# Kernel tuning notes

Measured on AMD Instinct MI355X. Metric: run time of the kernel, lower is better.

The kernel has to match this reference:

```python
import jax, jax.numpy as jnp
import numpy as np

N, E, H, B = 100000, 1600000, 64, 256
EPS = 1e-5


def ln(x, g, b):
    mu = jnp.mean(x, axis=-1, keepdims=True)
    var = jnp.mean((x - mu) ** 2, axis=-1, keepdims=True)
    return (x - mu) * jax.lax.rsqrt(var + EPS) * g + b


def gelu(x):
    # torch nn.GELU default is exact (erf) gelu
    return jax.nn.gelu(x, approximate=False)


def setup_inputs() -> dict:
    key = jax.random.key(0)
    ks = iter(jax.random.split(key, 64))
    nk = lambda: next(ks)
    s = 0.1
    p = {}
    p["x"] = jax.random.normal(nk(), (N, 2), jnp.float32)
    p["edge_attr"] = jax.random.normal(nk(), (E, 2), jnp.float32)
    # node_embed: Linear(2,H) LN GELU Linear(H,H) LN GELU (dropout = eval no-op)
    p["ne_w1"] = jax.random.normal(nk(), (2, H), jnp.float32) * s
    p["ne_b1"] = jnp.zeros((H,), jnp.float32)
    p["ne_g1"] = jnp.ones((H,), jnp.float32)
    p["ne_be1"] = jnp.zeros((H,), jnp.float32)
    p["ne_w2"] = jax.random.normal(nk(), (H, H), jnp.float32) * s
    p["ne_b2"] = jnp.zeros((H,), jnp.float32)
    p["ne_g2"] = jnp.ones((H,), jnp.float32)
    p["ne_be2"] = jnp.zeros((H,), jnp.float32)
    # 3 TrackConv layers: message MLP Linear(H+2,H)+LN, conv output LN, and outer per-layer LN
    p["conv_w"] = jax.random.normal(nk(), (3, H + 2, H), jnp.float32) * s
    p["conv_b"] = jnp.zeros((3, H), jnp.float32)
    p["conv_mg"] = jnp.ones((3, H), jnp.float32)
    p["conv_mb"] = jnp.zeros((3, H), jnp.float32)
    p["conv_ng"] = jnp.ones((3, H), jnp.float32)
    p["conv_nb"] = jnp.zeros((3, H), jnp.float32)
    p["out_ng"] = jnp.ones((3, H), jnp.float32)
    p["out_nb"] = jnp.zeros((3, H), jnp.float32)
    # head MLP: Linear(H,H)+LN+ReLU, Linear(H,H//2)+LN+ReLU, Linear(H//2,1)
    p["m_w1"] = jax.random.normal(nk(), (H, H), jnp.float32) * s
    p["m_b1"] = jnp.zeros((H,), jnp.float32)
    p["m_g1"] = jnp.ones((H,), jnp.float32)
    p["m_be1"] = jnp.zeros((H,), jnp.float32)
    p["m_w2"] = jax.random.normal(nk(), (H, H // 2), jnp.float32) * s
    p["m_b2"] = jnp.zeros((H // 2,), jnp.float32)
    p["m_g2"] = jnp.ones((H // 2,), jnp.float32)
    p["m_be2"] = jnp.zeros((H // 2,), jnp.float32)
    p["m_w3"] = jax.random.normal(nk(), (H // 2, 1), jnp.float32) * s
    p["m_b3"] = jnp.zeros((1,), jnp.float32)
    p["edge_index"] = jax.random.randint(nk(), (2, E), 0, N, dtype=jnp.int32)
    p["batch"] = jnp.sort(jax.random.randint(nk(), (N,), 0, B, dtype=jnp.int32))
    return p


def reference(x, edge_attr,
              ne_w1, ne_b1, ne_g1, ne_be1, ne_w2, ne_b2, ne_g2, ne_be2,
              conv_w, conv_b, conv_mg, conv_mb, conv_ng, conv_nb, out_ng, out_nb,
              m_w1, m_b1, m_g1, m_be1, m_w2, m_b2, m_g2, m_be2, m_w3, m_b3,
              edge_index, batch):
    # node embedding (dropout in eval = identity)
    h = gelu(ln(x @ ne_w1 + ne_b1, ne_g1, ne_be1))
    h = gelu(ln(h @ ne_w2 + ne_b2, ne_g2, ne_be2))
    src, dst = edge_index[0], edge_index[1]  # PyG: message from src (x_j), aggregate at dst
    deg = jax.ops.segment_sum(jnp.ones((E,), h.dtype), dst, num_segments=N)
    deg = jnp.maximum(deg, 1.0)[:, None]
    for l in range(3):
        msg_in = jnp.concatenate([h[src], edge_attr], axis=-1)  # [E, H+2]
        msg = gelu(ln(msg_in @ conv_w[l] + conv_b[l], conv_mg[l], conv_mb[l]))  # [E, H]
        agg = jax.ops.segment_sum(msg, dst, num_segments=N) / deg  # mean aggregate
        conv_out = ln(agg + h, conv_ng[l], conv_nb[l])  # TrackConv: norm(out + residual)
        h = h + ln(conv_out, out_ng[l], out_nb[l])  # outer norm + residual
    # global mean pool over graphs
    cnt = jnp.maximum(jax.ops.segment_sum(jnp.ones((N,), h.dtype), batch, num_segments=B), 1.0)[:, None]
    g = jax.ops.segment_sum(h, batch, num_segments=B) / cnt  # [B, H]
    g = jax.nn.relu(ln(g @ m_w1 + m_b1, m_g1, m_be1))
    g = jax.nn.relu(ln(g @ m_w2 + m_b2, m_g2, m_be2))
    return g @ m_w3 + m_b3  # [B, 1]
```

## Files before the change

kernel.cpp:

```cpp
#include <hip/hip_runtime.h>
#include <math.h>


typedef __attribute__((ext_vector_type(8))) short bfrag;
typedef __attribute__((ext_vector_type(4))) float ffrag;

template <int CTRL>
__device__ __forceinline__ float dpp_mov(float v) {
  return __int_as_float(
      __builtin_amdgcn_update_dpp(0, __float_as_int(v), CTRL, 0xF, 0xF, true));
}

__device__ __forceinline__ float rsum16(float v) {
  v += dpp_mov<0x128>(v);
  v += dpp_mov<0x124>(v);
  v += dpp_mov<0x122>(v);
  v += dpp_mov<0x121>(v);
  return v;
}

__device__ __forceinline__ float wave_sum64(float v) {
  v = rsum16(v);
  v += __shfl_xor(v, 16, 64);
  v += __shfl_xor(v, 32, 64);
  return v;
}

__device__ __forceinline__ float ln_apply(float t, float g, float b) {
  float s1 = wave_sum64(t);
  float s2 = wave_sum64(t * t);
  float mu = s1 * 0.015625f;
  float var = fmaf(-mu, mu, s2 * 0.015625f);
  return (t - mu) * rsqrtf(var + 1e-5f) * g + b;
}

__device__ __forceinline__ float erf_fast(float x) {
  float ax = fabsf(x);
  float p = fmaf(fmaf(fmaf(fmaf(0.078108f, ax, 0.000972f), ax, 0.230389f),
                      ax, 0.278393f), ax, 1.0f);
  p = p * p;
  p = p * p;
  float r = __builtin_amdgcn_rcpf(p);
  return copysignf(1.0f - r, x);
}

__device__ __forceinline__ float gelu_exact(float v) {
  float half = 0.5f * v;
  return fmaf(half, erf_fast(v * 0.70710678118654752440f), half);
}

__device__ __forceinline__ float lane_bcast(float v, int k) {
  return __uint_as_float(__builtin_amdgcn_readlane(__float_as_uint(v), k));
}

__device__ __forceinline__ short f2bf(float f) {
  union { float f; unsigned u; } v; v.f = f;
  unsigned r = v.u + 0x7fffu + ((v.u >> 16) & 1u);
  return (short)(r >> 16);
}

__global__ __launch_bounds__(256) void k_init(
    const float* __restrict__ x,
    const float* __restrict__ w1, const float* __restrict__ b1,
    const float* __restrict__ g1, const float* __restrict__ be1,
    const float* __restrict__ w2, const float* __restrict__ b2,
    const float* __restrict__ g2, const float* __restrict__ be2,
    const float* __restrict__ conv_w, ushort* __restrict__ wt,
    const int* __restrict__ ei, int* __restrict__ csr,
    float* __restrict__ h, ushort* __restrict__ hb,
    int n_nodes, int ne, int oHist, int oEmb, int embWaves) {
  const int bid = blockIdx.x;
  const int tid = threadIdx.x;
  if (bid < oHist) {
    const int i = bid * 256 + tid;
    const int k = i % 96, f = (i / 96) % 64, l = i / (96 * 64);
    const float v = (k < 66) ? conv_w[(size_t)l * 66 * 64 + k * 64 + f] : 0.0f;
    wt[i] = (ushort)f2bf(v);
    return;
  }
  if (bid < oEmb) {
    const int i = (bid - oHist) * 256 + tid;
    if (i < ne) atomicAdd(&csr[ei[ne + i]], 1);
    return;
  }
  const int lane = tid & 63;
  const int wid = ((bid - oEmb) * 256 + tid) >> 6;
  const int nw = embWaves;
  float wc[64];
#pragma unroll
  for (int k = 0; k < 64; k++) wc[k] = w2[k * 64 + lane];
  const float w1a = w1[lane], w1b = w1[64 + lane];
  const float vb1 = b1[lane], vg1 = g1[lane], vbe1 = be1[lane];
  const float vb2 = b2[lane], vg2 = g2[lane], vbe2 = be2[lane];
  for (int n = wid; n < n_nodes; n += nw) {
    const float x0 = x[2 * n], x1 = x[2 * n + 1];
    float t = fmaf(x0, w1a, fmaf(x1, w1b, vb1));
    t = gelu_exact(ln_apply(t, vg1, vbe1));
    float a0 = vb2, a1 = 0.f, a2 = 0.f, a3 = 0.f;
#pragma unroll
    for (int k = 0; k < 64; k += 4) {
      a0 = fmaf(lane_bcast(t, k + 0), wc[k + 0], a0);
      a1 = fmaf(lane_bcast(t, k + 1), wc[k + 1], a1);
      a2 = fmaf(lane_bcast(t, k + 2), wc[k + 2], a2);
      a3 = fmaf(lane_bcast(t, k + 3), wc[k + 3], a3);
    }
    float acc = (a0 + a1) + (a2 + a3);
    acc = gelu_exact(ln_apply(acc, vg2, vbe2));
    h[n * 64 + lane] = acc;
    hb[n * 64 + lane] = (ushort)f2bf(acc);
  }
}

__global__ __launch_bounds__(1024) void k_scan_fast(int* __restrict__ buf, int n) {
  __shared__ int wsum[16];
  const int tid = threadIdx.x, lane = tid & 63, w = tid >> 6;
  const int chunk = (((n + 1023) / 1024) + 3) & ~3;
  const int a = min(tid * chunk, n), b = min(a + chunk, n);
  const bool full = (a + chunk <= n);
  int s = 0;
  if (full) {
    const int4* p4 = (const int4*)(buf + a);
#pragma unroll 4
    for (int i = 0; i < chunk / 4; i++) {
      int4 v = p4[i];
      s += v.x + v.y + v.z + v.w;
    }
  } else {
    for (int i = a; i < b; i++) s += buf[i];
  }
  int inc = s;
#pragma unroll
  for (int sh = 1; sh < 64; sh <<= 1) {
    int t = __shfl_up(inc, sh, 64);
    if (lane >= sh) inc += t;
  }
  if (lane == 63) wsum[w] = inc;
  __syncthreads();
  int wb = 0;
  for (int j = 0; j < w; j++) wb += wsum[j];
  int excl = wb + inc - s;
  if (full) {
    int4* p4 = (int4*)(buf + a);
#pragma unroll 4
    for (int i = 0; i < chunk / 4; i++) {
      int4 v = p4[i];
      int4 o;
      o.x = excl; excl += v.x;
      o.y = excl; excl += v.y;
      o.z = excl; excl += v.z;
      o.w = excl; excl += v.w;
      p4[i] = o;
    }
  } else {
    for (int i = a; i < b; i++) { int v = buf[i]; buf[i] = excl; excl += v; }
  }
}

__global__ void k_scatter(const int* __restrict__ ei, const float* __restrict__ ea,
                          int* __restrict__ cursor, int2* __restrict__ edata, int ne) {
  int i = blockIdx.x * blockDim.x + threadIdx.x;
  if (i < ne) {
    const int d = ei[ne + i];
    const int s = ei[i];
    const float2 eav = *(const float2*)(ea + 2 * (size_t)i);
    const unsigned pk = (unsigned)(ushort)f2bf(eav.x) |
                        ((unsigned)(ushort)f2bf(eav.y) << 16);
    const int pos = atomicAdd(&cursor[d], 1);
    edata[pos] = make_int2(s, (int)pk);
  }
}

__global__ __launch_bounds__(256, 3) void k_edge_node(
    const float* __restrict__ h_in, const ushort* __restrict__ hb_in,
    float* __restrict__ h_out, ushort* __restrict__ hb_out,
    const int2* __restrict__ edata, const int* __restrict__ ends,
    const ushort* __restrict__ wt,
    const float* __restrict__ bias, const float* __restrict__ mg,
    const float* __restrict__ mb,
    const float* __restrict__ ng, const float* __restrict__ nb,
    const float* __restrict__ og, const float* __restrict__ ob,
    int n_nodes, int writeHb) {
  __shared__ __align__(16) ushort lwt[64 * 96];
  {
    const uint4* s = (const uint4*)wt;
    uint4* d = (uint4*)lwt;
    for (int i = threadIdx.x; i < 768; i += 256) d[i] = s[i];
  }
  __syncthreads();

  const int lane = threadIdx.x & 63;
  const int grp = lane >> 4, col = lane & 15;
  const int wid = (blockIdx.x * blockDim.x + threadIdx.x) >> 6;
  const int nw = (gridDim.x * blockDim.x) >> 6;

  float vb[4], vg[4], vbb[4];
#pragma unroll
  for (int t = 0; t < 4; t++) {
    const int f = t * 16 + col;
    vb[t] = bias[f]; vg[t] = mg[f]; vbb[t] = mb[f];
  }

  for (int n = wid; n < n_nodes; n += nw) {
    int start, end;
    if (n == 0) {
      start = 0; end = ends[0];
    } else {
      const int2 se = *(const int2*)(ends + n - 1);
      start = se.x; end = se.y;
    }
    float aggf[4] = {0.f, 0.f, 0.f, 0.f};

    int p = start;
    int2 ed = edata[p + min(col, end - p - 1)];
    const ushort* hp0 = hb_in + (size_t)ed.x * 64 + grp * 8;
    bfrag A0 = *(const bfrag*)(hp0);
    bfrag A1 = *(const bfrag*)(hp0 + 32);
    int edy = ed.y;

    for (;;) {
      const int rem = min(16, end - p);
      const int pn = p + 16;
      const bool more = pn < end;
      const int nidx = more ? (pn + min(col, end - pn - 1)) : (p + min(col, rem - 1));
      const int2 edn = edata[nidx];

      bfrag A2 = {0, 0, 0, 0, 0, 0, 0, 0};
      if (grp == 0) {
        A2[0] = (short)(edy & 0xffff);
        A2[1] = (short)((unsigned)edy >> 16);
      }

      ffrag acc[4];
#pragma unroll
      for (int t = 0; t < 4; t++) { ffrag c = {vb[t], vb[t], vb[t], vb[t]}; acc[t] = c; }
#pragma unroll
      for (int t = 0; t < 4; t++) {
        const bfrag B = *(const bfrag*)(lwt + (t * 16 + col) * 96 + grp * 8);
        acc[t] = __builtin_amdgcn_mfma_f32_16x16x32_bf16(A0, B, acc[t], 0, 0, 0);
      }
#pragma unroll
      for (int t = 0; t < 4; t++) {
        const bfrag B = *(const bfrag*)(lwt + (t * 16 + col) * 96 + 32 + grp * 8);
        acc[t] = __builtin_amdgcn_mfma_f32_16x16x32_bf16(A1, B, acc[t], 0, 0, 0);
      }
#pragma unroll
      for (int t = 0; t < 4; t++) {
        const bfrag B = *(const bfrag*)(lwt + (t * 16 + col) * 96 + 64 + grp * 8);
        acc[t] = __builtin_amdgcn_mfma_f32_16x16x32_bf16(A2, B, acc[t], 0, 0, 0);
      }

      const ushort* hq = hb_in + (size_t)edn.x * 64 + grp * 8;
      const bfrag N0 = *(const bfrag*)(hq);
      const bfrag N1 = *(const bfrag*)(hq + 32);

      float sx[4], sq[4];
#pragma unroll
      for (int r = 0; r < 4; r++) {
        float s = (acc[0][r] + acc[1][r]) + (acc[2][r] + acc[3][r]);
        float q = fmaf(acc[0][r], acc[0][r], fmaf(acc[1][r], acc[1][r],
                  fmaf(acc[2][r], acc[2][r], acc[3][r] * acc[3][r])));
        sx[r] = s; sq[r] = q;
      }
#pragma unroll
      for (int r = 0; r < 4; r++) sx[r] = rsum16(sx[r]);
#pragma unroll
      for (int r = 0; r < 4; r++) sq[r] = rsum16(sq[r]);
      float iv[4], mi[4], mk[4];
#pragma unroll
      for (int r = 0; r < 4; r++) {
        const float mu = sx[r] * 0.015625f;
        const float var = fmaf(-mu, mu, sq[r] * 0.015625f);
        iv[r] = rsqrtf(var + 1e-5f);
        mi[r] = -mu * iv[r];
        mk[r] = (grp * 4 + r < rem) ? 1.0f : 0.0f;
      }

#pragma unroll
      for (int t = 0; t < 4; t++) {
        float rs = 0.f;
#pragma unroll
        for (int r = 0; r < 4; r++) {
          const float z = fmaf(acc[t][r], iv[r], mi[r]);
          float v = fmaf(z, vg[t], vbb[t]);
          v = gelu_exact(v);
          rs = fmaf(v, mk[r], rs);
        }
        aggf[t] += rs;
      }

      if (!more) break;
      p = pn; A0 = N0; A1 = N1; edy = edn.y;
    }

#pragma unroll
    for (int t = 0; t < 4; t++) {
      float v = aggf[t];
      v += __shfl_xor(v, 16, 64);
      v += __shfl_xor(v, 32, 64);
      aggf[t] = v;
    }

    const float aggl = (grp == 0) ? aggf[0] : (grp == 1) ? aggf[1]
                     : (grp == 2) ? aggf[2] : aggf[3];

    const float dg = fmaxf((float)(end - start), 1.0f);
    const float hv = h_in[(size_t)n * 64 + lane];
    const float a = aggl / dg + hv;
    const float c = ln_apply(a, ng[lane], nb[lane]);
    const float o = ln_apply(c, og[lane], ob[lane]);
    const float outv = hv + o;
    h_out[(size_t)n * 64 + lane] = outv;
    if (writeHb) hb_out[(size_t)n * 64 + lane] = (ushort)f2bf(outv);
  }
}

__global__ void k_pool_seg(const float* __restrict__ h, const int* __restrict__ batch,
                           float* __restrict__ g, float* __restrict__ cnt,
                           int n_nodes, int chunk) {
  const int lane = threadIdx.x & 63;
  const int wid = (blockIdx.x * blockDim.x + threadIdx.x) >> 6;
  const int n0 = wid * chunk;
  if (n0 >= n_nodes) return;
  const int n1 = min(n0 + chunk, n_nodes);
  int cur = batch[n0], c = 0;
  float acc = 0.f;
  for (int n = n0; n < n1; n++) {
    const int b = batch[n];
    if (b != cur) {
      atomicAdd(&g[(size_t)cur * 64 + lane], acc);
      if (lane == 0) atomicAdd(&cnt[cur], (float)c);
      acc = 0.f; c = 0; cur = b;
    }
    acc += h[(size_t)n * 64 + lane];
    c++;
  }
  atomicAdd(&g[(size_t)cur * 64 + lane], acc);
  if (lane == 0) atomicAdd(&cnt[cur], (float)c);
}

__global__ void k_head(const float* __restrict__ g, const float* __restrict__ cnt,
                       const float* __restrict__ w1, const float* __restrict__ b1,
                       const float* __restrict__ g1, const float* __restrict__ be1,
                       const float* __restrict__ w2, const float* __restrict__ b2,
                       const float* __restrict__ g2, const float* __restrict__ be2,
                       const float* __restrict__ w3, const float* __restrict__ b3,
                       float* __restrict__ out, int nb_) {
  const int lane = threadIdx.x & 63;
  const int row = (blockIdx.x * blockDim.x + threadIdx.x) >> 6;
  if (row >= nb_) return;
  const float c = fmaxf(cnt[row], 1.0f);
  const float gv = g[row * 64 + lane] / c;
  float a0 = b1[lane], a1 = 0.f, a2 = 0.f, a3 = 0.f;
#pragma unroll
  for (int k = 0; k < 64; k += 4) {
    a0 = fmaf(lane_bcast(gv, k + 0), w1[(k + 0) * 64 + lane], a0);
    a1 = fmaf(lane_bcast(gv, k + 1), w1[(k + 1) * 64 + lane], a1);
    a2 = fmaf(lane_bcast(gv, k + 2), w1[(k + 2) * 64 + lane], a2);
    a3 = fmaf(lane_bcast(gv, k + 3), w1[(k + 3) * 64 + lane], a3);
  }
  float t = (a0 + a1) + (a2 + a3);
  t = fmaxf(ln_apply(t, g1[lane], be1[lane]), 0.0f);

  const int j = lane & 31;
  float c0 = b2[j], c1 = 0.f, c2 = 0.f, c3 = 0.f;
#pragma unroll
  for (int k = 0; k < 64; k += 4) {
    c0 = fmaf(lane_bcast(t, k + 0), w2[(k + 0) * 32 + j], c0);
    c1 = fmaf(lane_bcast(t, k + 1), w2[(k + 1) * 32 + j], c1);
    c2 = fmaf(lane_bcast(t, k + 2), w2[(k + 2) * 32 + j], c2);
    c3 = fmaf(lane_bcast(t, k + 3), w2[(k + 3) * 32 + j], c3);
  }
  float t2 = (c0 + c1) + (c2 + c3);
  t2 = fmaxf(ln_apply(t2, g2[j], be2[j]), 0.0f);
  const float p = t2 * w3[j];
  const float s = wave_sum64(p) * 0.5f;
  if (lane == 0) out[row] = s + b3[0];
}

extern "C" void kernel_launch(void* const* d_in, const int* in_sizes, int n_in,
                              void* d_out, int out_size, void* d_ws, size_t ws_size,
                              hipStream_t stream) {
  const float* x      = (const float*)d_in[0];
  const float* ea     = (const float*)d_in[1];
  const float* ne_w1  = (const float*)d_in[2];
  const float* ne_b1  = (const float*)d_in[3];
  const float* ne_g1  = (const float*)d_in[4];
  const float* ne_be1 = (const float*)d_in[5];
  const float* ne_w2  = (const float*)d_in[6];
  const float* ne_b2  = (const float*)d_in[7];
  const float* ne_g2  = (const float*)d_in[8];
  const float* ne_be2 = (const float*)d_in[9];
  const float* conv_w = (const float*)d_in[10];
  const float* conv_b = (const float*)d_in[11];
  const float* conv_mg= (const float*)d_in[12];
  const float* conv_mb= (const float*)d_in[13];
  const float* conv_ng= (const float*)d_in[14];
  const float* conv_nb= (const float*)d_in[15];
  const float* out_ng = (const float*)d_in[16];
  const float* out_nb = (const float*)d_in[17];
  const float* m_w1   = (const float*)d_in[18];
  const float* m_b1   = (const float*)d_in[19];
  const float* m_g1   = (const float*)d_in[20];
  const float* m_be1  = (const float*)d_in[21];
  const float* m_w2   = (const float*)d_in[22];
  const float* m_b2   = (const float*)d_in[23];
  const float* m_g2   = (const float*)d_in[24];
  const float* m_be2  = (const float*)d_in[25];
  const float* m_w3   = (const float*)d_in[26];
  const float* m_b3   = (const float*)d_in[27];
  const int*   eidx   = (const int*)d_in[28];
  const int*   batch  = (const int*)d_in[29];
  float* outp = (float*)d_out;

  const int NN = in_sizes[29];
  const int NE = in_sizes[1] / 2;
  const int NB = out_size;

  float* ws = (float*)d_ws;
  float*  h0   = ws;
  float*  h1   = h0 + (size_t)NN * 64;
  float*  gbuf = h1 + (size_t)NN * 64;
  float*  cnt  = gbuf + (size_t)NB * 64;
  int*    csr  = (int*)(cnt + NB);
  ushort* wt   = (ushort*)(csr + NN);
  ushort* hb0  = wt + 3 * 64 * 96;
  ushort* hb1  = hb0 + (size_t)NN * 64;
  int2*   edata= (int2*)(hb1 + (size_t)NN * 64);

  const dim3 blk(256);

  hipMemsetAsync(gbuf, 0, sizeof(float) * ((size_t)NB * 64 + NB) +
                          sizeof(int) * (size_t)NN, stream);

  const int nPrep = (3 * 64 * 96) / 256;
  const int nHist = (NE + 255) / 256;
  const int oHist = nPrep, oEmb = nPrep + nHist;
  const int embBlocks = 2048;
  k_init<<<oEmb + embBlocks, blk, 0, stream>>>(
      x, ne_w1, ne_b1, ne_g1, ne_be1, ne_w2, ne_b2, ne_g2, ne_be2,
      conv_w, wt, eidx, csr, h0, hb0, NN, NE, oHist, oEmb, embBlocks * 4);

  k_scan_fast<<<1, 1024, 0, stream>>>(csr, NN);
  k_scatter<<<(NE + 255) / 256, blk, 0, stream>>>(eidx, ea, csr, edata, NE);

  float* hin = h0;  float* hout = h1;
  ushort* hbin = hb0; ushort* hbout = hb1;
  for (int l = 0; l < 3; l++) {
    k_edge_node<<<4096, blk, 0, stream>>>(
        hin, hbin, hout, hbout, edata, csr, wt + (size_t)l * 64 * 96,
        conv_b + l * 64, conv_mg + l * 64, conv_mb + l * 64,
        conv_ng + l * 64, conv_nb + l * 64,
        out_ng + l * 64, out_nb + l * 64, NN, (l < 2) ? 1 : 0);
    float* tf = hin; hin = hout; hout = tf;
    ushort* tb = hbin; hbin = hbout; hbout = tb;
  }

  {
    const int chunk = 32;
    const int nwaves = (NN + chunk - 1) / chunk;
    const int nblocks = (nwaves * 64 + 255) / 256;
    k_pool_seg<<<nblocks, blk, 0, stream>>>(hin, batch, gbuf, cnt, NN, chunk);
  }
  k_head<<<(NB + 3) / 4, blk, 0, stream>>>(gbuf, cnt, m_w1, m_b1, m_g1, m_be1,
                                           m_w2, m_b2, m_g2, m_be2, m_w3, m_b3,
                                           outp, NB);
}
```

Measured before the change: 817.4 us.

## Split edge-node kernel into edge-balanced chunked messaging with atomic aggregation

Replaces the per-destination-node wave loop with fixed 16-edge chunks over the dst-sorted edge list. Segments inside each chunk are reduced and atomically added into an fp32 aggregate buffer, and a separate node-update kernel then applies the mean, the two layernorms and the residual, and re-zeroes the buffer. This is meant to remove load imbalance and partial-tile waste from variable node degrees. In exchange it adds float atomics, an extra launch per layer, wider edge records (int4 with dst), and a nondeterministic summation order.

New measurement: 766.2 us. -6.3%, faster.

```diff
diff --git a/kernel.cpp b/kernel.cpp
--- a/kernel.cpp
+++ b/kernel.cpp
@@ -157,7 +157,7 @@
 }
 
 __global__ void k_scatter(const int* __restrict__ ei, const float* __restrict__ ea,
-                          int* __restrict__ cursor, int2* __restrict__ edata, int ne) {
+                          int* __restrict__ cursor, int4* __restrict__ edata, int ne) {
   int i = blockIdx.x * blockDim.x + threadIdx.x;
   if (i < ne) {
     const int d = ei[ne + i];
@@ -166,20 +166,15 @@
     const unsigned pk = (unsigned)(ushort)f2bf(eav.x) |
                         ((unsigned)(ushort)f2bf(eav.y) << 16);
     const int pos = atomicAdd(&cursor[d], 1);
-    edata[pos] = make_int2(s, (int)pk);
-  }
-}
-
-__global__ __launch_bounds__(256, 3) void k_edge_node(
-    const float* __restrict__ h_in, const ushort* __restrict__ hb_in,
-    float* __restrict__ h_out, ushort* __restrict__ hb_out,
-    const int2* __restrict__ edata, const int* __restrict__ ends,
-    const ushort* __restrict__ wt,
+    edata[pos] = make_int4(s, (int)pk, d, 0);
+  }
+}
+
+__global__ __launch_bounds__(256, 3) void k_edge_packed(
+    const ushort* __restrict__ hb_in, float* __restrict__ agg,
+    const int4* __restrict__ edata, const ushort* __restrict__ wt,
     const float* __restrict__ bias, const float* __restrict__ mg,
-    const float* __restrict__ mb,
-    const float* __restrict__ ng, const float* __restrict__ nb,
-    const float* __restrict__ og, const float* __restrict__ ob,
-    int n_nodes, int writeHb) {
+    const float* __restrict__ mb, int nchunks, int ne) {
   __shared__ __align__(16) ushort lwt[64 * 96];
   {
     const uint4* s = (const uint4*)wt;
@@ -200,118 +195,134 @@
     vb[t] = bias[f]; vg[t] = mg[f]; vbb[t] = mb[f];
   }
 
-  for (int n = wid; n < n_nodes; n += nw) {
-    int start, end;
-    if (n == 0) {
-      start = 0; end = ends[0];
-    } else {
-      const int2 se = *(const int2*)(ends + n - 1);
-      start = se.x; end = se.y;
-    }
-    float aggf[4] = {0.f, 0.f, 0.f, 0.f};
-
-    int p = start;
-    int2 ed = edata[p + min(col, end - p - 1)];
-    const ushort* hp0 = hb_in + (size_t)ed.x * 64 + grp * 8;
-    bfrag A0 = *(const bfrag*)(hp0);
-    bfrag A1 = *(const bfrag*)(hp0 + 32);
-    int edy = ed.y;
-
-    for (;;) {
-      const int rem = min(16, end - p);
-      const int pn = p + 16;
-      const bool more = pn < end;
-      const int nidx = more ? (pn + min(col, end - pn - 1)) : (p + min(col, rem - 1));
-      const int2 edn = edata[nidx];
-
-      bfrag A2 = {0, 0, 0, 0, 0, 0, 0, 0};
-      if (grp == 0) {
-        A2[0] = (short)(edy & 0xffff);
-        A2[1] = (short)((unsigned)edy >> 16);
+  int c = wid;
+  if (c >= nchunks) return;
+  int4 e = edata[min(16 * c + col, ne - 1)];
+  {
+    const ushort* hp = hb_in + (size_t)e.x * 64 + grp * 8;
+  }
+  const ushort* hp0 = hb_in + (size_t)e.x * 64 + grp * 8;
+  bfrag A0 = *(const bfrag*)(hp0);
+  bfrag A1 = *(const bfrag*)(hp0 + 32);
+
+  for (;;) {
+    const int rem = min(16, ne - 16 * c);
+    const int cn = c + nw;
+    const bool more = cn < nchunks;
+    const int nslot = more ? min(16 * cn + col, ne - 1) : min(16 * c + col, ne - 1);
+    const int4 en = edata[nslot];
+
+    bfrag A2 = {0, 0, 0, 0, 0, 0, 0, 0};
+    if (grp == 0) {
+      A2[0] = (short)(e.y & 0xffff);
+      A2[1] = (short)((unsigned)e.y >> 16);
+    }
+
+    ffrag acc[4];
+#pragma unroll
+    for (int t = 0; t < 4; t++) { ffrag cc = {vb[t], vb[t], vb[t], vb[t]}; acc[t] = cc; }
+#pragma unroll
+    for (int t = 0; t < 4; t++) {
+      const bfrag B = *(const bfrag*)(lwt + (t * 16 + col) * 96 + grp * 8);
+      acc[t] = __builtin_amdgcn_mfma_f32_16x16x32_bf16(A0, B, acc[t], 0, 0, 0);
+    }
+#pragma unroll
+    for (int t = 0; t < 4; t++) {
+      const bfrag B = *(const bfrag*)(lwt + (t * 16 + col) * 96 + 32 + grp * 8);
+      acc[t] = __builtin_amdgcn_mfma_f32_16x16x32_bf16(A1, B, acc[t], 0, 0, 0);
+    }
+#pragma unroll
+    for (int t = 0; t < 4; t++) {
+      const bfrag B = *(const bfrag*)(lwt + (t * 16 + col) * 96 + 64 + grp * 8);
+      acc[t] = __builtin_amdgcn_mfma_f32_16x16x32_bf16(A2, B, acc[t], 0, 0, 0);
+    }
+
+    const ushort* hq = hb_in + (size_t)en.x * 64 + grp * 8;
+    const bfrag N0 = *(const bfrag*)(hq);
+    const bfrag N1 = *(const bfrag*)(hq + 32);
+
+    float sx[4], sq[4];
+#pragma unroll
+    for (int r = 0; r < 4; r++) {
+      float s = (acc[0][r] + acc[1][r]) + (acc[2][r] + acc[3][r]);
+      float q = fmaf(acc[0][r], acc[0][r], fmaf(acc[1][r], acc[1][r],
+                fmaf(acc[2][r], acc[2][r], acc[3][r] * acc[3][r])));
+      sx[r] = s; sq[r] = q;
+    }
+#pragma unroll
+    for (int r = 0; r < 4; r++) sx[r] = rsum16(sx[r]);
+#pragma unroll
+    for (int r = 0; r < 4; r++) sq[r] = rsum16(sq[r]);
+    float iv[4], mi[4];
+#pragma unroll
+    for (int r = 0; r < 4; r++) {
+      const float mu = sx[r] * 0.015625f;
+      const float var = fmaf(-mu, mu, sq[r] * 0.015625f);
+      iv[r] = rsqrtf(var + 1e-5f);
+      mi[r] = -mu * iv[r];
+    }
+
+#pragma unroll
+    for (int t = 0; t < 4; t++) {
+#pragma unroll
+      for (int r = 0; r < 4; r++) {
+        const float z = fmaf(acc[t][r], iv[r], mi[r]);
+        acc[t][r] = gelu_exact(fmaf(z, vg[t], vbb[t]));
       }
-
-      ffrag acc[4];
-#pragma unroll
-      for (int t = 0; t < 4; t++) { ffrag c = {vb[t], vb[t], vb[t], vb[t]}; acc[t] = c; }
-#pragma unroll
-      for (int t = 0; t < 4; t++) {
-        const bfrag B = *(const bfrag*)(lwt + (t * 16 + col) * 96 + grp * 8);
-        acc[t] = __builtin_amdgcn_mfma_f32_16x16x32_bf16(A0, B, acc[t], 0, 0, 0);
-      }
-#pragma unroll
-      for (int t = 0; t < 4; t++) {
-        const bfrag B = *(const bfrag*)(lwt + (t * 16 + col) * 96 + 32 + grp * 8);
-        acc[t] = __builtin_amdgcn_mfma_f32_16x16x32_bf16(A1, B, acc[t], 0, 0, 0);
-      }
-#pragma unroll
-      for (int t = 0; t < 4; t++) {
-        const bfrag B = *(const bfrag*)(lwt + (t * 16 + col) * 96 + 64 + grp * 8);
-        acc[t] = __builtin_amdgcn_mfma_f32_16x16x32_bf16(A2, B, acc[t], 0, 0, 0);
-      }
-
-      const ushort* hq = hb_in + (size_t)edn.x * 64 + grp * 8;
-      const bfrag N0 = *(const bfrag*)(hq);
-      const bfrag N1 = *(const bfrag*)(hq + 32);
-
-      float sx[4], sq[4];
-#pragma unroll
-      for (int r = 0; r < 4; r++) {
-        float s = (acc[0][r] + acc[1][r]) + (acc[2][r] + acc[3][r]);
-        float q = fmaf(acc[0][r], acc[0][r], fmaf(acc[1][r], acc[1][r],
-                  fmaf(acc[2][r], acc[2][r], acc[3][r] * acc[3][r])));
-        sx[r] = s; sq[r] = q;
-      }
-#pragma unroll
-      for (int r = 0; r < 4; r++) sx[r] = rsum16(sx[r]);
-#pragma unroll
-      for (int r = 0; r < 4; r++) sq[r] = rsum16(sq[r]);
-      float iv[4], mi[4], mk[4];
-#pragma unroll
-      for (int r = 0; r < 4; r++) {
-        const float mu = sx[r] * 0.015625f;
-        const float var = fmaf(-mu, mu, sq[r] * 0.015625f);
-        iv[r] = rsqrtf(var + 1e-5f);
-        mi[r] = -mu * iv[r];
-        mk[r] = (grp * 4 + r < rem) ? 1.0f : 0.0f;
-      }
-
+    }
+
+    const int prev = __shfl_up(e.z, 1, 64);
+    const unsigned long long bal = __ballot((col > 0) && (e.z != prev));
+    const unsigned bm = (unsigned)bal & 0xFFFEu;
+
+    int s0 = 0;
+    while (s0 < rem) {
+      const unsigned rest = bm >> (s0 + 1);
+      int s1 = rest ? (s0 + 1 + __builtin_ctz(rest)) : 16;
+      if (s1 > rem) s1 = rem;
+      const int dseg = __builtin_amdgcn_readlane(e.z, s0);
 #pragma unroll
       for (int t = 0; t < 4; t++) {
         float rs = 0.f;
 #pragma unroll
         for (int r = 0; r < 4; r++) {
-          const float z = fmaf(acc[t][r], iv[r], mi[r]);
-          float v = fmaf(z, vg[t], vbb[t]);
-          v = gelu_exact(v);
-          rs = fmaf(v, mk[r], rs);
+          const int row = grp * 4 + r;
+          const float w = (row >= s0 && row < s1) ? 1.0f : 0.0f;
+          rs = fmaf(acc[t][r], w, rs);
         }
-        aggf[t] += rs;
+        rs += __shfl_xor(rs, 16, 64);
+        rs += __shfl_xor(rs, 32, 64);
+        if (lane < 16)
+          atomicAdd(&agg[(size_t)dseg * 64 + t * 16 + lane], rs);
       }
-
-      if (!more) break;
-      p = pn; A0 = N0; A1 = N1; edy = edn.y;
-    }
-
-#pragma unroll
-    for (int t = 0; t < 4; t++) {
-      float v = aggf[t];
-      v += __shfl_xor(v, 16, 64);
-      v += __shfl_xor(v, 32, 64);
-      aggf[t] = v;
-    }
-
-    const float aggl = (grp == 0) ? aggf[0] : (grp == 1) ? aggf[1]
-                     : (grp == 2) ? aggf[2] : aggf[3];
-
-    const float dg = fmaxf((float)(end - start), 1.0f);
-    const float hv = h_in[(size_t)n * 64 + lane];
-    const float a = aggl / dg + hv;
-    const float c = ln_apply(a, ng[lane], nb[lane]);
-    const float o = ln_apply(c, og[lane], ob[lane]);
-    const float outv = hv + o;
-    h_out[(size_t)n * 64 + lane] = outv;
-    if (writeHb) hb_out[(size_t)n * 64 + lane] = (ushort)f2bf(outv);
-  }
+      s0 = s1;
+    }
+
+    if (!more) break;
+    c = cn; e = en; A0 = N0; A1 = N1;
+  }
+}
+
+__global__ void k_node_update(float* __restrict__ h, ushort* __restrict__ hb,
+                              float* __restrict__ agg, const int* __restrict__ ends,
+                              const float* __restrict__ ng, const float* __restrict__ nb,
+                              const float* __restrict__ og, const float* __restrict__ ob,
+                              int n_nodes, int writeHb) {
+  const int lane = threadIdx.x & 63;
+  const int n = (blockIdx.x * blockDim.x + threadIdx.x) >> 6;
+  if (n >= n_nodes) return;
+  int start, end;
+  if (n == 0) { start = 0; end = ends[0]; }
+  else { const int2 se = *(const int2*)(ends + n - 1); start = se.x; end = se.y; }
+  const float dg = fmaxf((float)(end - start), 1.0f);
+  const float hv = h[(size_t)n * 64 + lane];
+  const float a = agg[(size_t)n * 64 + lane] / dg + hv;
+  if (writeHb) agg[(size_t)n * 64 + lane] = 0.0f;
+  const float c = ln_apply(a, ng[lane], nb[lane]);
+  const float o = ln_apply(c, og[lane], ob[lane]);
+  const float outv = hv + o;
+  h[(size_t)n * 64 + lane] = outv;
+  if (writeHb) hb[(size_t)n * 64 + lane] = (ushort)f2bf(outv);
 }
 
 __global__ void k_pool_seg(const float* __restrict__ h, const int* __restrict__ batch,
@@ -415,22 +426,23 @@
   const int NN = in_sizes[29];
   const int NE = in_sizes[1] / 2;
   const int NB = out_size;
-
-  float* ws = (float*)d_ws;
-  float*  h0   = ws;
-  float*  h1   = h0 + (size_t)NN * 64;
-  float*  gbuf = h1 + (size_t)NN * 64;
+  const int NCH = (NE + 15) / 16;
+
+  char* wsb = (char*)d_ws;
+  float*  h    = (float*)wsb;
+  ushort* hb   = (ushort*)(h + (size_t)NN * 64);
+  int4*   edata= (int4*)((char*)hb + ((size_t)NN * 128 + 15) / 16 * 16);
+  ushort* wt   = (ushort*)(edata + NE);
+  float*  gbuf = (float*)(wt + 3 * 64 * 96);
   float*  cnt  = gbuf + (size_t)NB * 64;
   int*    csr  = (int*)(cnt + NB);
-  ushort* wt   = (ushort*)(csr + NN);
-  ushort* hb0  = wt + 3 * 64 * 96;
-  ushort* hb1  = hb0 + (size_t)NN * 64;
-  int2*   edata= (int2*)(hb1 + (size_t)NN * 64);
+  float*  agg  = (float*)((char*)(csr + NN) +
+                          (((size_t)(uintptr_t)(csr + NN) & 15) ? 16 - ((size_t)(uintptr_t)(csr + NN) & 15) : 0));
 
   const dim3 blk(256);
 
-  hipMemsetAsync(gbuf, 0, sizeof(float) * ((size_t)NB * 64 + NB) +
-                          sizeof(int) * (size_t)NN, stream);
+  const size_t zbytes = (char*)(agg + (size_t)NN * 64) - (char*)gbuf;
+  hipMemsetAsync(gbuf, 0, zbytes, stream);
 
   const int nPrep = (3 * 64 * 96) / 256;
   const int nHist = (NE + 255) / 256;
@@ -438,28 +450,25 @@
   const int embBlocks = 2048;
   k_init<<<oEmb + embBlocks, blk, 0, stream>>>(
       x, ne_w1, ne_b1, ne_g1, ne_be1, ne_w2, ne_b2, ne_g2, ne_be2,
-      conv_w, wt, eidx, csr, h0, hb0, NN, NE, oHist, oEmb, embBlocks * 4);
+      conv_w, wt, eidx, csr, h, hb, NN, NE, oHist, oEmb, embBlocks * 4);
 
   k_scan_fast<<<1, 1024, 0, stream>>>(csr, NN);
   k_scatter<<<(NE + 255) / 256, blk, 0, stream>>>(eidx, ea, csr, edata, NE);
 
-  float* hin = h0;  float* hout = h1;
-  ushort* hbin = hb0; ushort* hbout = hb1;
   for (int l = 0; l < 3; l++) {
-    k_edge_node<<<4096, blk, 0, stream>>>(
-        hin, hbin, hout, hbout, edata, csr, wt + (size_t)l * 64 * 96,
-        conv_b + l * 64, conv_mg + l * 64, conv_mb + l * 64,
-        conv_ng + l * 64, conv_nb + l * 64,
+    k_edge_packed<<<4096, blk, 0, stream>>>(
+        hb, agg, edata, wt + (size_t)l * 64 * 96,
+        conv_b + l * 64, conv_mg + l * 64, conv_mb + l * 64, NCH, NE);
+    k_node_update<<<(NN * 64 + 255) / 256, blk, 0, stream>>>(
+        h, hb, agg, csr, conv_ng + l * 64, conv_nb + l * 64,
         out_ng + l * 64, out_nb + l * 64, NN, (l < 2) ? 1 : 0);
-    float* tf = hin; hin = hout; hout = tf;
-    ushort* tb = hbin; hbin = hbout; hbout = tb;
   }
 
   {
     const int chunk = 32;
     const int nwaves = (NN + chunk - 1) / chunk;
     const int nblocks = (nwaves * 64 + 255) / 256;
-    k_pool_seg<<<nblocks, blk, 0, stream>>>(hin, batch, gbuf, cnt, NN, chunk);
+    k_pool_seg<<<nblocks, blk, 0, stream>>>(h, batch, gbuf, cnt, NN, chunk);
   }
   k_head<<<(NB + 3) / 4, blk, 0, stream>>>(gbuf, cnt, m_w1, m_b1, m_g1, m_be1,
                                            m_w2, m_b2, m_g2, m_be2, m_w3, m_b3,
```
